# Kernel optimization log

Hardware: AMD Instinct MI355X
Metric: run time of the kernel (lower is better)

## Reference

```python
import jax, jax.numpy as jnp
import numpy as np

T, B, N_IN, N_RNN = 205, 2048, 33, 256
ALPHA = 0.2        # hp['dt']/hp['tau'] = 20/100
SIGMA_REC = 0.0    # hp['sigma_rec'] = 0 -> noise term vanishes


def setup_inputs() -> dict:
    key = jax.random.key(0)
    k_x, k_w = jax.random.split(key)
    x = jax.random.normal(k_x, (T, B, N_IN), dtype=jnp.float32)
    # kernel = concat([w_in (N_IN,N_RNN), w_rec (N_RNN,N_RNN)]) along axis 0
    kernel = jax.random.normal(k_w, (N_IN + N_RNN, N_RNN), dtype=jnp.float32)
    kernel = kernel / np.float32(np.sqrt(N_IN + N_RNN))  # keep dynamics stable
    bias = jnp.zeros((N_RNN,), dtype=jnp.float32)
    h0 = jnp.zeros((B, N_RNN), dtype=jnp.float32)
    return {"x": x, "kernel": kernel, "bias": bias, "h0": h0}


def reference(x, kernel, bias, h0):
    # Leaky RNN cell (Yang et al. style):
    #   gate = concat([x_t, h]) @ kernel + bias
    #   act  = relu(gate + noise)          (noise = sqrt(2*alpha)*sigma_rec*randn; sigma_rec=0)
    #   h    = (1 - alpha) * h + alpha * act
    def step(h, x_t):
        pre = jnp.concatenate([x_t, h], axis=-1) @ kernel + bias  # [B, N_RNN]
        h_new = (1.0 - ALPHA) * h + ALPHA * jax.nn.relu(pre)
        return h_new, h_new

    _, hs = jax.lax.scan(step, h0, x)  # hs: [T, B, N_RNN]
    return hs
```

## Files before the change

### kernel.cpp

```cpp
#include <hip/hip_runtime.h>
#include <cstddef>

#define T_STEPS 205
#define BATCH   2048
#define NIN     33
#define NRNN    256
#define BB      8
#define NTHREADS 512
#define NTW     2


#define A_STRIDE  264
#define X_BSTRIDE 32
#define X_TSTRIDE (BB * X_BSTRIDE)
#define WS_STRIDE 40

typedef _Float16 half8 __attribute__((ext_vector_type(8)));
typedef float    f32x4 __attribute__((ext_vector_type(4)));
typedef unsigned int uintx2 __attribute__((ext_vector_type(2)));

__device__ __forceinline__ void lds_barrier() {
    asm volatile("s_waitcnt lgkmcnt(0)\n\ts_barrier" ::: "memory");
}

__device__ __forceinline__ float permlane_merge(float a, float b) {
    uintx2 r = __builtin_amdgcn_permlane32_swap(
        __builtin_bit_cast(unsigned int, a),
        __builtin_bit_cast(unsigned int, b), false, false);
    return __builtin_bit_cast(float, r[0]);
}

__device__ __forceinline__ int grow(int kk) {
    return (kk < NRNN) ? (33 + kk) : (kk - NRNN);
}

__global__ __launch_bounds__(NTHREADS, 1)
void leaky_rnn_kernel(const float* __restrict__ x,
                      const float* __restrict__ W,
                      const float* __restrict__ bias,
                      const float* __restrict__ h0,
                      float* __restrict__ out)
{
    __shared__ __align__(16) _Float16 A_lds[2][8 * A_STRIDE];
    __shared__ __align__(16) _Float16 X_lds[T_STEPS * X_TSTRIDE];
    __shared__ __align__(16) float    X32[T_STEPS * BB];

    const int tid  = threadIdx.x;
    const int lane = tid & 63;
    const int wave = tid >> 6;
    const int q    = lane >> 4;
    const int nlo  = lane & 15;
    const int qe   = q & 1;
    const int hi   = lane >> 5;
    const int b0   = blockIdx.x * BB;

    _Float16* Wst = &X_lds[0];
    half8 wfrag[NTW][9];
    {
        const int c   = tid & 255;
        const int oct = tid >> 8;
        #pragma unroll
        for (int kt = 0; kt < 9; ++kt) {
            __syncthreads();
            #pragma unroll
            for (int o2 = 0; o2 < 2; ++o2) {
                int o = oct + 2 * o2;
                half8 pack;
                #pragma unroll
                for (int i = 0; i < 8; ++i)
                    pack[i] = (_Float16)W[grow(kt * 32 + o * 8 + i) * NRNN + c];
                *(half8*)&Wst[c * WS_STRIDE + o * 8] = pack;
            }
            __syncthreads();
            #pragma unroll
            for (int nt = 0; nt < NTW; ++nt) {
                int n = wave * 32 + nt * 16 + nlo;
                wfrag[nt][kt] = *(const half8*)&Wst[n * WS_STRIDE + q * 8];
            }
        }
        __syncthreads();
    }

    const int   ecol = wave * 32 + hi * 16 + nlo;
    const float bve  = bias[ecol];
    const float w32e = W[32 * NRNN + ecol];

    for (int e = tid; e < T_STEPS * (BB * NIN); e += NTHREADS) {
        int t  = e / (BB * NIN);
        int i  = e - t * (BB * NIN);
        int b  = i / NIN;
        int xi = i - b * NIN;
        float v = x[(size_t)t * (BATCH * NIN) + (size_t)b0 * NIN + i];
        if (xi < 32) X_lds[t * X_TSTRIDE + b * X_BSTRIDE + xi] = (_Float16)v;
        else         X32[t * BB + b] = v;
    }

    float hreg[4];
    #pragma unroll
    for (int r = 0; r < 4; ++r) {
        int b = qe * 4 + r;
        float h = h0[(b0 + b) * NRNN + ecol];
        hreg[r] = h;
        A_lds[0][b * A_STRIDE + ecol] = (_Float16)h;
    }
    __syncthreads();

    const int am = nlo & 7;
    half8 xf   = *(const half8*)&X_lds[am * X_BSTRIDE + q * 8];
    f32x4 x32v = *(const f32x4*)&X32[qe * 4];

    int p = 0;
    for (int t = 0; t < T_STEPS; ++t) {
        const _Float16* __restrict__ Ar = A_lds[p];
        _Float16* __restrict__ Aw = A_lds[p ^ 1];

        f32x4 acc[NTW][2];
        #pragma unroll
        for (int nt = 0; nt < NTW; ++nt)
            #pragma unroll
            for (int s = 0; s < 2; ++s) acc[nt][s] = (f32x4){0.f, 0.f, 0.f, 0.f};

        #pragma unroll
        for (int kt = 0; kt < 8; ++kt) {
            half8 af = *(const half8*)&Ar[am * A_STRIDE + kt * 32 + q * 8];
            acc[0][kt & 1] = __builtin_amdgcn_mfma_f32_16x16x32_f16(af, wfrag[0][kt], acc[0][kt & 1], 0, 0, 0);
            acc[1][kt & 1] = __builtin_amdgcn_mfma_f32_16x16x32_f16(af, wfrag[1][kt], acc[1][kt & 1], 0, 0, 0);
        }
        acc[0][0] = __builtin_amdgcn_mfma_f32_16x16x32_f16(xf, wfrag[0][8], acc[0][0], 0, 0, 0);
        acc[1][0] = __builtin_amdgcn_mfma_f32_16x16x32_f16(xf, wfrag[1][8], acc[1][0], 0, 0, 0);

        f32x4 s0 = acc[0][0] + acc[0][1];
        f32x4 s1 = acc[1][0] + acc[1][1];

        float hn_[4];
        #pragma unroll
        for (int r = 0; r < 4; ++r) {
            float m   = permlane_merge(s0[r], s1[r]);
            float pre = m + bve + x32v[r] * w32e;
            float hn  = 0.8f * hreg[r] + 0.2f * fmaxf(pre, 0.f);
            hreg[r] = hn;
            hn_[r]  = hn;
            Aw[(qe * 4 + r) * A_STRIDE + ecol] = (_Float16)hn;
        }

        const int tn = (t + 1 < T_STEPS) ? (t + 1) : t;
        half8 xf_n   = *(const half8*)&X_lds[tn * X_TSTRIDE + am * X_BSTRIDE + q * 8];
        f32x4 x32v_n = *(const f32x4*)&X32[tn * BB + qe * 4];

        float* op = out + ((size_t)t * BATCH + b0 + qe * 4) * NRNN + ecol;
        #pragma unroll
        for (int r = 0; r < 4; ++r)
            __builtin_nontemporal_store(hn_[r], op + (size_t)r * NRNN);

        lds_barrier();
        xf = xf_n; x32v = x32v_n;
        p ^= 1;
    }
}

extern "C" void kernel_launch(void* const* d_in, const int* in_sizes, int n_in,
                              void* d_out, int out_size, void* d_ws, size_t ws_size,
                              hipStream_t stream) {
    const float* x    = (const float*)d_in[0];
    const float* W    = (const float*)d_in[1];
    const float* bias = (const float*)d_in[2];
    const float* h0   = (const float*)d_in[3];
    float* out = (float*)d_out;

    dim3 grid(BATCH / BB);
    dim3 block(NTHREADS);
    leaky_rnn_kernel<<<grid, block, 0, stream>>>(x, W, bias, h0, out);
}
```

Baseline: 546.5 us.

## Halve block to 4 waves, each computing 64 columns with 4 N-tiles

Reduces the workgroup from 8 to 4 waves, with each wave holding weight fragments for 64 output columns (four 16-wide N tiles) instead of 32. Each A fragment read from LDS now feeds four MFMAs per k-step, and the per-step barrier synchronizes fewer waves. The x staging now uses float4 global loads, and the x fragment is loaded at the start of each step instead of being prefetched during the previous one. The trade-off is more VGPRs for the weight fragments and a longer serial MFMA chain per wave, giving less latency hiding on the recurrent critical path.

```diff
diff --git a/kernel.cpp b/kernel.cpp
--- a/kernel.cpp
+++ b/kernel.cpp
@@ -6,8 +6,8 @@
 #define NIN     33
 #define NRNN    256
 #define BB      8
-#define NTHREADS 512
-#define NTW     2
+#define NTHREADS 256
+#define NTW     4
 
 
 #define A_STRIDE  264
@@ -57,14 +57,12 @@
     _Float16* Wst = &X_lds[0];
     half8 wfrag[NTW][9];
     {
-        const int c   = tid & 255;
-        const int oct = tid >> 8;
+        const int c = tid;
         #pragma unroll
         for (int kt = 0; kt < 9; ++kt) {
             __syncthreads();
             #pragma unroll
-            for (int o2 = 0; o2 < 2; ++o2) {
-                int o = oct + 2 * o2;
+            for (int o = 0; o < 4; ++o) {
                 half8 pack;
                 #pragma unroll
                 for (int i = 0; i < 8; ++i)
@@ -74,45 +72,56 @@
             __syncthreads();
             #pragma unroll
             for (int nt = 0; nt < NTW; ++nt) {
-                int n = wave * 32 + nt * 16 + nlo;
+                int n = wave * 64 + nt * 16 + nlo;
                 wfrag[nt][kt] = *(const half8*)&Wst[n * WS_STRIDE + q * 8];
             }
         }
         __syncthreads();
     }
 
-    const int   ecol = wave * 32 + hi * 16 + nlo;
-    const float bve  = bias[ecol];
-    const float w32e = W[32 * NRNN + ecol];
-
-    for (int e = tid; e < T_STEPS * (BB * NIN); e += NTHREADS) {
-        int t  = e / (BB * NIN);
-        int i  = e - t * (BB * NIN);
-        int b  = i / NIN;
-        int xi = i - b * NIN;
-        float v = x[(size_t)t * (BATCH * NIN) + (size_t)b0 * NIN + i];
-        if (xi < 32) X_lds[t * X_TSTRIDE + b * X_BSTRIDE + xi] = (_Float16)v;
-        else         X32[t * BB + b] = v;
+    int ecol[2]; float bve[2]; float w32e[2];
+    #pragma unroll
+    for (int p2 = 0; p2 < 2; ++p2) {
+        ecol[p2] = wave * 64 + (2 * p2 + hi) * 16 + nlo;
+        bve[p2]  = bias[ecol[p2]];
+        w32e[p2] = W[32 * NRNN + ecol[p2]];
     }
 
-    float hreg[4];
+    for (int e = tid; e < T_STEPS * 66; e += NTHREADS) {
+        int t  = e / 66;
+        int r4 = e - t * 66;
+        f32x4 v = *(const f32x4*)&x[((size_t)t * BATCH + b0) * NIN + r4 * 4];
+        #pragma unroll
+        for (int j = 0; j < 4; ++j) {
+            int idx = r4 * 4 + j;
+            int b   = idx / 33;
+            int xi  = idx - b * 33;
+            if (xi < 32) X_lds[t * X_TSTRIDE + b * X_BSTRIDE + xi] = (_Float16)v[j];
+            else         X32[t * BB + b] = v[j];
+        }
+    }
+
+    float hreg[2][4];
     #pragma unroll
-    for (int r = 0; r < 4; ++r) {
-        int b = qe * 4 + r;
-        float h = h0[(b0 + b) * NRNN + ecol];
-        hreg[r] = h;
-        A_lds[0][b * A_STRIDE + ecol] = (_Float16)h;
-    }
+    for (int p2 = 0; p2 < 2; ++p2)
+        #pragma unroll
+        for (int r = 0; r < 4; ++r) {
+            int b = qe * 4 + r;
+            float h = h0[(b0 + b) * NRNN + ecol[p2]];
+            hreg[p2][r] = h;
+            A_lds[0][b * A_STRIDE + ecol[p2]] = (_Float16)h;
+        }
     __syncthreads();
 
     const int am = nlo & 7;
-    half8 xf   = *(const half8*)&X_lds[am * X_BSTRIDE + q * 8];
-    f32x4 x32v = *(const f32x4*)&X32[qe * 4];
-
     int p = 0;
     for (int t = 0; t < T_STEPS; ++t) {
         const _Float16* __restrict__ Ar = A_lds[p];
         _Float16* __restrict__ Aw = A_lds[p ^ 1];
+        const _Float16* __restrict__ Xt = &X_lds[t * X_TSTRIDE];
+
+        half8 xf   = *(const half8*)&Xt[am * X_BSTRIDE + q * 8];
+        f32x4 x32v = *(const f32x4*)&X32[t * BB + qe * 4];
 
         f32x4 acc[NTW][2];
         #pragma unroll
@@ -123,37 +132,40 @@
         #pragma unroll
         for (int kt = 0; kt < 8; ++kt) {
             half8 af = *(const half8*)&Ar[am * A_STRIDE + kt * 32 + q * 8];
-            acc[0][kt & 1] = __builtin_amdgcn_mfma_f32_16x16x32_f16(af, wfrag[0][kt], acc[0][kt & 1], 0, 0, 0);
-            acc[1][kt & 1] = __builtin_amdgcn_mfma_f32_16x16x32_f16(af, wfrag[1][kt], acc[1][kt & 1], 0, 0, 0);
+            #pragma unroll
+            for (int nt = 0; nt < NTW; ++nt)
+                acc[nt][kt & 1] = __builtin_amdgcn_mfma_f32_16x16x32_f16(af, wfrag[nt][kt], acc[nt][kt & 1], 0, 0, 0);
         }
-        acc[0][0] = __builtin_amdgcn_mfma_f32_16x16x32_f16(xf, wfrag[0][8], acc[0][0], 0, 0, 0);
-        acc[1][0] = __builtin_amdgcn_mfma_f32_16x16x32_f16(xf, wfrag[1][8], acc[1][0], 0, 0, 0);
+        #pragma unroll
+        for (int nt = 0; nt < NTW; ++nt)
+            acc[nt][0] = __builtin_amdgcn_mfma_f32_16x16x32_f16(xf, wfrag[nt][8], acc[nt][0], 0, 0, 0);
 
-        f32x4 s0 = acc[0][0] + acc[0][1];
-        f32x4 s1 = acc[1][0] + acc[1][1];
+        f32x4 s[NTW];
+        #pragma unroll
+        for (int nt = 0; nt < NTW; ++nt) s[nt] = acc[nt][0] + acc[nt][1];
 
-        float hn_[4];
+        float hn_[2][4];
         #pragma unroll
-        for (int r = 0; r < 4; ++r) {
-            float m   = permlane_merge(s0[r], s1[r]);
-            float pre = m + bve + x32v[r] * w32e;
-            float hn  = 0.8f * hreg[r] + 0.2f * fmaxf(pre, 0.f);
-            hreg[r] = hn;
-            hn_[r]  = hn;
-            Aw[(qe * 4 + r) * A_STRIDE + ecol] = (_Float16)hn;
+        for (int p2 = 0; p2 < 2; ++p2)
+            #pragma unroll
+            for (int r = 0; r < 4; ++r) {
+                float m   = permlane_merge(s[2 * p2][r], s[2 * p2 + 1][r]);
+                float pre = m + bve[p2] + x32v[r] * w32e[p2];
+                float hn  = 0.8f * hreg[p2][r] + 0.2f * fmaxf(pre, 0.f);
+                hreg[p2][r] = hn;
+                hn_[p2][r]  = hn;
+                Aw[(qe * 4 + r) * A_STRIDE + ecol[p2]] = (_Float16)hn;
+            }
+
+        #pragma unroll
+        for (int p2 = 0; p2 < 2; ++p2) {
+            float* op = out + ((size_t)t * BATCH + b0 + qe * 4) * NRNN + ecol[p2];
+            #pragma unroll
+            for (int r = 0; r < 4; ++r)
+                __builtin_nontemporal_store(hn_[p2][r], op + (size_t)r * NRNN);
         }
 
-        const int tn = (t + 1 < T_STEPS) ? (t + 1) : t;
-        half8 xf_n   = *(const half8*)&X_lds[tn * X_TSTRIDE + am * X_BSTRIDE + q * 8];
-        f32x4 x32v_n = *(const f32x4*)&X32[tn * BB + qe * 4];
-
-        float* op = out + ((size_t)t * BATCH + b0 + qe * 4) * NRNN + ecol;
-        #pragma unroll
-        for (int r = 0; r < 4; ++r)
-            __builtin_nontemporal_store(hn_[r], op + (size_t)r * NRNN);
-
         lds_barrier();
-        xf = xf_n; x32v = x32v_n;
         p ^= 1;
     }
 }
```

After: 562.5 us. 1.03x slower.
